# Optimization experiments

Measured on AMD Instinct MI355X. Metric: run time of the kernel, lower is better.

The kernel has to match this reference:

```python
import jax, jax.numpy as jnp
import numpy as np

NUM_HEADS = 32
NUM_KV_HEADS = 8
HEAD_DIM = 128
ROPE_THETA = 10000.0


def _rope_cos_sin(seq_len, head_dim, dtype):
    inv_freq = 1.0 / (ROPE_THETA ** (jnp.arange(0, head_dim, 2, dtype=jnp.float32) / head_dim))
    t = jnp.arange(seq_len, dtype=jnp.float32)
    freqs = jnp.outer(t, inv_freq)              # [S, hd/2]
    emb = jnp.concatenate([freqs, freqs], axis=-1)  # [S, hd]
    return jnp.cos(emb).astype(dtype), jnp.sin(emb).astype(dtype)


def _rotate_half(x):
    h = x.shape[-1] // 2
    return jnp.concatenate([-x[..., h:], x[..., :h]], axis=-1)


def _apply_rope(x, cos, sin):
    # x: [B, H, S, D]; cos/sin: [S, D] (position_ids = arange(S) in prefill)
    return x * cos[None, None] + _rotate_half(x) * sin[None, None]


def setup_inputs() -> dict:
    key = jax.random.key(0)
    ks = jax.random.split(key, 5)
    B, S, H = 1, 2048, 4096
    return {
        "hidden_states": jax.random.normal(ks[0], (B, S, H), dtype=jnp.float32),
        "Wq": jax.random.normal(ks[1], (H, NUM_HEADS * HEAD_DIM), dtype=jnp.float32) * 0.02,
        "Wk": jax.random.normal(ks[2], (H, NUM_KV_HEADS * HEAD_DIM), dtype=jnp.float32) * 0.02,
        "Wv": jax.random.normal(ks[3], (H, NUM_KV_HEADS * HEAD_DIM), dtype=jnp.float32) * 0.02,
        "Wo": jax.random.normal(ks[4], (NUM_HEADS * HEAD_DIM, H), dtype=jnp.float32) * 0.02,
    }


def reference(hidden_states, Wq, Wk, Wv, Wo):
    B, S, H = hidden_states.shape
    nh, nkv, hd = NUM_HEADS, NUM_KV_HEADS, HEAD_DIM
    groups = nh // nkv

    # fused QKV projections (bias-free, Llama-style)
    q = (hidden_states @ Wq).reshape(B, S, nh, hd).transpose(0, 2, 1, 3)   # [B,nh,S,D]
    k = (hidden_states @ Wk).reshape(B, S, nkv, hd).transpose(0, 2, 1, 3)  # [B,nkv,S,D]
    v = (hidden_states @ Wv).reshape(B, S, nkv, hd).transpose(0, 2, 1, 3)

    # inline RoPE on q and k
    cos, sin = _rope_cos_sin(S, hd, q.dtype)
    q = _apply_rope(q, cos, sin)
    k = _apply_rope(k, cos, sin)

    # GQA: repeat kv heads to match query heads (num_key_value_groups)
    k = jnp.repeat(k, groups, axis=1)  # [B,nh,S,D]
    v = jnp.repeat(v, groups, axis=1)

    scale = 1.0 / jnp.sqrt(jnp.asarray(hd, dtype=q.dtype))
    logits = jnp.einsum("bhqd,bhkd->bhqk", q, k) * scale  # [B,nh,S,S]

    # prefill causal mask (phys_past_len = 0)
    causal = jnp.tril(jnp.ones((S, S), dtype=bool))
    neg = jnp.asarray(jnp.finfo(logits.dtype).min, dtype=logits.dtype)
    logits = jnp.where(causal[None, None], logits, neg)

    attn = jax.nn.softmax(logits.astype(jnp.float32), axis=-1).astype(q.dtype)
    out = jnp.einsum("bhqk,bhkd->bhqd", attn, v)           # [B,nh,S,D]
    out = out.transpose(0, 2, 1, 3).reshape(B, S, nh * hd)  # [B,S,H]
    return out @ Wo
```

## Files before the change

### kernel.cpp

```cpp
#include <hip/hip_runtime.h>
#include <cstdint>
#include <cstddef>

typedef __attribute__((ext_vector_type(4))) float f32x4;
typedef __attribute__((ext_vector_type(16))) float f32x16;
typedef __attribute__((ext_vector_type(8))) short bf16x8;
typedef __attribute__((ext_vector_type(2))) unsigned int u32x2;

#define S_LEN   2048
#define HID     4096
#define NH      32
#define NKV     8
#define HD      128
#define QKV_N   6144

typedef const __attribute__((address_space(1))) unsigned int* gptr_t;
typedef __attribute__((address_space(3))) unsigned int* lptr_t;

__device__ __forceinline__ void gload_lds16(const void* g, void* l) {
  __builtin_amdgcn_global_load_lds((gptr_t)g, (lptr_t)l, 16, 0, 0);
}

__device__ __forceinline__ ushort f2bf(float f) {
  union { float f; uint32_t u; } v; v.f = f;
  uint32_t r = v.u + 0x7FFFu + ((v.u >> 16) & 1u);
  return (ushort)(r >> 16);
}
__device__ __forceinline__ float bf2f(ushort u) {
  union { uint32_t u; float f; } v; v.u = ((uint32_t)u) << 16;
  return v.f;
}

__global__ void prep_all(const float* __restrict__ hs,
                         const float* __restrict__ Wq, const float* __restrict__ Wk,
                         const float* __restrict__ Wv, const float* __restrict__ Wo,
                         ushort* __restrict__ hsb,
                         ushort* __restrict__ WqkvT, ushort* __restrict__ WoT) {
  int id = blockIdx.x;
  if (id < 8192) {
    int i = (id * 256 + (int)threadIdx.x) * 4;
    float4 v = *reinterpret_cast<const float4*>(hs + i);
    ushort4 o;
    o.x = f2bf(v.x); o.y = f2bf(v.y); o.z = f2bf(v.z); o.w = f2bf(v.w);
    *reinterpret_cast<ushort4*>(hsb + i) = o;
    return;
  }
  __shared__ float t[32][33];
  id -= 8192;
  const float* src; ushort* dst; int C, local;
  if (id < 16384)        { src = Wq; dst = WqkvT;                      C = 4096; local = id; }
  else if (id < 20480)   { src = Wk; dst = WqkvT + (size_t)4096 * HID; C = 1024; local = id - 16384; }
  else if (id < 24576)   { src = Wv; dst = WqkvT + (size_t)5120 * HID; C = 1024; local = id - 20480; }
  else                   { src = Wo; dst = WoT;                        C = 4096; local = id - 24576; }
  const int cb = C >> 5;
  int bx = local % cb, by = local / cb;
  int tx = threadIdx.x & 31, ty = threadIdx.x >> 5;
  int r0 = by * 32, c0 = bx * 32;
#pragma unroll
  for (int i = 0; i < 32; i += 8)
    t[ty + i][tx] = src[(size_t)(r0 + ty + i) * C + c0 + tx];
  __syncthreads();
#pragma unroll
  for (int i = 0; i < 32; i += 8)
    dst[(size_t)(c0 + ty + i) * 4096 + r0 + tx] = f2bf(t[tx][ty + i]);
}

template <bool BF16_OUT>
__global__ __launch_bounds__(256, 4) void gemm_bt(
    const ushort* __restrict__ A, const ushort* __restrict__ B,
    void* __restrict__ Cp, int M, int N, int K) {
  __shared__ ushort a_lds[128 * 64];
  __shared__ ushort b_lds[128 * 64];
  const int tid = threadIdx.x;
  const int wid = tid >> 6, lane = tid & 63;
  const int l16 = lane & 15, lk = lane >> 4;
  const int wr = wid >> 1, wc = wid & 1;
  const size_t a_row0 = (size_t)blockIdx.y * 128;
  const size_t b_row0 = (size_t)blockIdx.x * 128;

  f32x4 acc[4][4] = {};

  for (int kt = 0; kt < K; kt += 64) {
    __syncthreads();
#pragma unroll
    for (int i = 0; i < 4; ++i) {
      int c = i * 256 + tid;
      int row = c >> 3, pos = c & 7;
      int src = pos ^ (row & 7);
      gload_lds16(A + (a_row0 + row) * K + kt + src * 8, &a_lds[c * 8]);
      gload_lds16(B + (b_row0 + row) * K + kt + src * 8, &b_lds[c * 8]);
    }
    __syncthreads();

#pragma unroll
    for (int kk = 0; kk < 2; ++kk) {
      bf16x8 af[4], bf[4];
#pragma unroll
      for (int m = 0; m < 4; ++m) {
        int row = wr * 64 + m * 16 + l16;
        int ch = (kk * 4 + lk) ^ (row & 7);
        af[m] = *reinterpret_cast<const bf16x8*>(&a_lds[row * 64 + ch * 8]);
      }
#pragma unroll
      for (int n = 0; n < 4; ++n) {
        int row = wc * 64 + n * 16 + l16;
        int ch = (kk * 4 + lk) ^ (row & 7);
        bf[n] = *reinterpret_cast<const bf16x8*>(&b_lds[row * 64 + ch * 8]);
      }
#pragma unroll
      for (int m = 0; m < 4; ++m)
#pragma unroll
        for (int n = 0; n < 4; ++n)
          acc[m][n] = __builtin_amdgcn_mfma_f32_16x16x32_bf16(af[m], bf[n], acc[m][n], 0, 0, 0);
    }
  }

#pragma unroll
  for (int m = 0; m < 4; ++m) {
    int row_b = wr * 64 + m * 16 + lk * 4;
#pragma unroll
    for (int n = 0; n < 4; ++n) {
      int col = (int)b_row0 + wc * 64 + n * 16 + l16;
#pragma unroll
      for (int r = 0; r < 4; ++r) {
        size_t row = a_row0 + row_b + r;
        if constexpr (BF16_OUT)
          ((ushort*)Cp)[row * N + col] = f2bf(acc[m][n][r]);
        else
          ((float*)Cp)[row * N + col] = acc[m][n][r];
      }
    }
  }
}

__global__ __launch_bounds__(256, 4) void gemm_o_ks(
    const ushort* __restrict__ A, const ushort* __restrict__ B,
    float* __restrict__ P0, float* __restrict__ P1) {
  __shared__ ushort a_lds[128 * 64];
  __shared__ ushort b_lds[128 * 64];
  const int bid = blockIdx.x;
  const int kh = bid >> 9;
  const int rem = bid & 511;
  const size_t b_row0 = (size_t)(rem & 31) * 128;
  const size_t a_row0 = (size_t)(rem >> 5) * 128;
  const int k0 = kh * 2048, k1 = k0 + 2048;
  float* __restrict__ P = kh ? P1 : P0;
  const int tid = threadIdx.x;
  const int wid = tid >> 6, lane = tid & 63;
  const int l16 = lane & 15, lk = lane >> 4;
  const int wr = wid >> 1, wc = wid & 1;

  f32x4 acc[4][4] = {};

  for (int kt = k0; kt < k1; kt += 64) {
    __syncthreads();
#pragma unroll
    for (int i = 0; i < 4; ++i) {
      int c = i * 256 + tid;
      int row = c >> 3, pos = c & 7;
      int src = pos ^ (row & 7);
      gload_lds16(A + (a_row0 + row) * HID + kt + src * 8, &a_lds[c * 8]);
      gload_lds16(B + (b_row0 + row) * HID + kt + src * 8, &b_lds[c * 8]);
    }
    __syncthreads();

#pragma unroll
    for (int kk = 0; kk < 2; ++kk) {
      bf16x8 af[4], bf[4];
#pragma unroll
      for (int m = 0; m < 4; ++m) {
        int row = wr * 64 + m * 16 + l16;
        int ch = (kk * 4 + lk) ^ (row & 7);
        af[m] = *reinterpret_cast<const bf16x8*>(&a_lds[row * 64 + ch * 8]);
      }
#pragma unroll
      for (int n = 0; n < 4; ++n) {
        int row = wc * 64 + n * 16 + l16;
        int ch = (kk * 4 + lk) ^ (row & 7);
        bf[n] = *reinterpret_cast<const bf16x8*>(&b_lds[row * 64 + ch * 8]);
      }
#pragma unroll
      for (int m = 0; m < 4; ++m)
#pragma unroll
        for (int n = 0; n < 4; ++n)
          acc[m][n] = __builtin_amdgcn_mfma_f32_16x16x32_bf16(af[m], bf[n], acc[m][n], 0, 0, 0);
    }
  }

#pragma unroll
  for (int m = 0; m < 4; ++m) {
    int row_b = wr * 64 + m * 16 + lk * 4;
#pragma unroll
    for (int n = 0; n < 4; ++n) {
      int col = (int)b_row0 + wc * 64 + n * 16 + l16;
#pragma unroll
      for (int r = 0; r < 4; ++r)
        P[(a_row0 + row_b + r) * HID + col] = acc[m][n][r];
    }
  }
}

__global__ void add_f32(const float* __restrict__ a, const float* __restrict__ b,
                        float* __restrict__ o, int n) {
  int i = (blockIdx.x * 256 + threadIdx.x) * 4;
  if (i >= n) return;
  float4 x = *reinterpret_cast<const float4*>(a + i);
  float4 y = *reinterpret_cast<const float4*>(b + i);
  float4 z; z.x = x.x + y.x; z.y = x.y + y.y; z.z = x.z + y.z; z.w = x.w + y.w;
  *reinterpret_cast<float4*>(o + i) = z;
}

__global__ void rope_and_tv(ushort* __restrict__ QKV, ushort* __restrict__ Vt) {
  if (blockIdx.x < 2560) {
    int idx = blockIdx.x * 256 + threadIdx.x;
    int dg = idx & 7;
    int t = idx >> 3;
    int s = t / 40;
    int hh = t - s * 40;
    if (s >= S_LEN) return;
    int col = (hh < NH) ? hh * HD : HID + (hh - NH) * HD;
    ushort* base = QKV + (size_t)s * QKV_N + col + dg * 8;

    union U { uint4 v; ushort u[8]; };
    U L, H, OL, OH;
    L.v = *reinterpret_cast<const uint4*>(base);
    H.v = *reinterpret_cast<const uint4*>(base + 64);
    const float C0 = 13.287712379549449f / 64.0f;
#pragma unroll
    for (int j = 0; j < 8; ++j) {
      int d = dg * 8 + j;
      float invf = exp2f(-(float)d * C0);
      float ang = (float)s * invf;
      float sn, cs;
      sincosf(ang, &sn, &cs);
      float xl = bf2f(L.u[j]), xh = bf2f(H.u[j]);
      OL.u[j] = f2bf(xl * cs - xh * sn);
      OH.u[j] = f2bf(xh * cs + xl * sn);
    }
    *reinterpret_cast<uint4*>(base) = OL.v;
    *reinterpret_cast<uint4*>(base + 64) = OH.v;
  } else {
    __shared__ ushort t[64][65];
    int local = blockIdx.x - 2560;
    int s0 = (local & 31) * 64;
    int d0 = ((local >> 5) & 1) * 64;
    int hkv = local >> 6;
    int tx = threadIdx.x & 63, ty = threadIdx.x >> 6;
#pragma unroll
    for (int i = 0; i < 64; i += 4)
      t[i + ty][tx] = QKV[(size_t)(s0 + i + ty) * QKV_N + HID + NKV * HD + hkv * HD + d0 + tx];
    __syncthreads();
#pragma unroll
    for (int i = 0; i < 64; i += 4)
      Vt[((size_t)hkv * HD + d0 + i + ty) * S_LEN + s0 + tx] = t[tx][i + ty];
  }
}

__global__ __launch_bounds__(256, 2) void attn_kernel(
    const ushort* __restrict__ QKV, const ushort* __restrict__ Vt, ushort* __restrict__ AO) {
  constexpr float SCALE = 0.08838834764831845f;
  __shared__ ushort k_lds[2][64 * 128];
  __shared__ ushort v_lds[2][128 * 64];

  const int lin = blockIdx.x;
  const int h = ((lin & 7) << 2) + ((lin >> 3) & 3);
  const int p = lin >> 5;
  const int hkv = h >> 2;
  const int tid = threadIdx.x, wid = tid >> 6, lane = tid & 63;
  const int l32 = lane & 31;
  const int hi = lane >> 5;

  auto stageKV = [&](int buf, int kt) {
#pragma unroll
    for (int i = 0; i < 4; ++i) {
      int c = i * 256 + wid * 64 + lane;
      int row = c >> 4, ch = c & 15;
      int sch = ch ^ (row & 7);
      gload_lds16(QKV + (size_t)(kt * 64 + row) * QKV_N + HID + hkv * HD + sch * 8,
                  &k_lds[buf][c * 8]);
    }
#pragma unroll
    for (int i = 0; i < 4; ++i) {
      int c = i * 256 + wid * 64 + lane;
      int row = c >> 3, ch = c & 7;
      int sch = ch ^ (row & 7);
      gload_lds16(Vt + ((size_t)hkv * HD + row) * S_LEN + (size_t)kt * 64 + sch * 8,
                  &v_lds[buf][c * 8]);
    }
  };

  for (int pi = 0; pi < 2; ++pi) {
    const int qb = pi ? (15 - p) : p;
    const int q0 = qb * 128;
    const int qg = q0 + wid * 32 + l32;

    bf16x8 qf[8];
    {
      const ushort* qrow = QKV + (size_t)qg * QKV_N + h * HD + hi * 8;
#pragma unroll
      for (int ds = 0; ds < 8; ++ds)
        qf[ds] = *reinterpret_cast<const bf16x8*>(qrow + ds * 16);
    }

    float m_run = -1e30f, l_run = 0.f;
    f32x16 oacc[4] = {};

    stageKV(0, 0);
    __syncthreads();

    const int nt = 2 * qb + 2;
    for (int kt = 0; kt < nt; ++kt) {
      const int cur = kt & 1;
      if (kt + 1 < nt) stageKV(cur ^ 1, kt + 1);

      if (kt * 64 <= q0 + wid * 32 + 31) {
        float pv[32];
        __builtin_amdgcn_s_setprio(1);
#pragma unroll
        for (int kf = 0; kf < 2; ++kf) {
          f32x16 s = {};
          int rk = kf * 32 + l32;
#pragma unroll
          for (int ds = 0; ds < 8; ++ds) {
            int c16 = (ds * 2 + hi) ^ (rk & 7);
            bf16x8 kfr = *reinterpret_cast<const bf16x8*>(&k_lds[cur][rk * 128 + c16 * 8]);
            s = __builtin_amdgcn_mfma_f32_32x32x16_bf16(kfr, qf[ds], s, 0, 0, 0);
          }
#pragma unroll
          for (int r = 0; r < 16; ++r) pv[kf * 16 + r] = s[r] * SCALE;
        }
        __builtin_amdgcn_s_setprio(0);

        if (kt * 64 + 63 > q0 + wid * 32) {
#pragma unroll
          for (int kf = 0; kf < 2; ++kf)
#pragma unroll
            for (int r = 0; r < 16; ++r) {
              int kl = kf * 32 + (r & 3) + 8 * (r >> 2) + 4 * hi;
              if (kt * 64 + kl > qg) pv[kf * 16 + r] = -1e30f;
            }
        }

        float mt = pv[0];
#pragma unroll
        for (int i = 1; i < 32; ++i) mt = fmaxf(mt, pv[i]);
        mt = fmaxf(mt, __shfl_xor(mt, 32, 64));
        float mn = fmaxf(m_run, mt);
        float alpha = __expf(m_run - mn);
        float ls = 0.f;
#pragma unroll
        for (int i = 0; i < 32; ++i) { pv[i] = __expf(pv[i] - mn); ls += pv[i]; }
        ls += __shfl_xor(ls, 32, 64);
        l_run = l_run * alpha + ls;
        m_run = mn;
#pragma unroll
        for (int f = 0; f < 4; ++f)
#pragma unroll
          for (int r = 0; r < 16; ++r) oacc[f][r] *= alpha;

        union PW { uint32_t w[4]; bf16x8 v; } pa[4];
#pragma unroll
        for (int ks = 0; ks < 4; ++ks) {
          uint32_t x0, x1, y0, y1;
          asm("v_cvt_pk_bf16_f32 %0, %1, %2" : "=v"(x0) : "v"(pv[8 * ks + 0]), "v"(pv[8 * ks + 1]));
          asm("v_cvt_pk_bf16_f32 %0, %1, %2" : "=v"(x1) : "v"(pv[8 * ks + 2]), "v"(pv[8 * ks + 3]));
          asm("v_cvt_pk_bf16_f32 %0, %1, %2" : "=v"(y0) : "v"(pv[8 * ks + 4]), "v"(pv[8 * ks + 5]));
          asm("v_cvt_pk_bf16_f32 %0, %1, %2" : "=v"(y1) : "v"(pv[8 * ks + 6]), "v"(pv[8 * ks + 7]));
          u32x2 r0 = __builtin_amdgcn_permlane32_swap(x0, y0, false, false);
          u32x2 r1 = __builtin_amdgcn_permlane32_swap(x1, y1, false, false);
          pa[ks].w[0] = r0.x; pa[ks].w[1] = r1.x; pa[ks].w[2] = r0.y; pa[ks].w[3] = r1.y;
        }

        __builtin_amdgcn_s_setprio(1);
#pragma unroll
        for (int ks = 0; ks < 4; ++ks) {
#pragma unroll
          for (int f = 0; f < 4; ++f) {
            int dv = f * 32 + l32;
            int c8 = (2 * ks + hi) ^ (dv & 7);
            bf16x8 vfr = *reinterpret_cast<const bf16x8*>(&v_lds[cur][dv * 64 + c8 * 8]);
            oacc[f] = __builtin_amdgcn_mfma_f32_32x32x16_bf16(vfr, pa[ks].v, oacc[f], 0, 0, 0);
          }
        }
        __builtin_amdgcn_s_setprio(0);
      }

      __syncthreads();
    }

    float inv_l = 1.0f / l_run;
    ushort* aorow = AO + (size_t)qg * HID + h * HD;
#pragma unroll
    for (int f = 0; f < 4; ++f)
#pragma unroll
      for (int g = 0; g < 4; ++g) {
        ushort4 o;
        o.x = f2bf(oacc[f][g * 4 + 0] * inv_l);
        o.y = f2bf(oacc[f][g * 4 + 1] * inv_l);
        o.z = f2bf(oacc[f][g * 4 + 2] * inv_l);
        o.w = f2bf(oacc[f][g * 4 + 3] * inv_l);
        *reinterpret_cast<ushort4*>(aorow + f * 32 + g * 8 + 4 * hi) = o;
      }
  }
}

extern "C" void kernel_launch(void* const* d_in, const int* in_sizes, int n_in,
                              void* d_out, int out_size, void* d_ws, size_t ws_size,
                              hipStream_t stream) {
  (void)in_sizes; (void)n_in; (void)out_size;
  const float* hs = (const float*)d_in[0];
  const float* Wq = (const float*)d_in[1];
  const float* Wk = (const float*)d_in[2];
  const float* Wv = (const float*)d_in[3];
  const float* Wo = (const float*)d_in[4];
  float* out = (float*)d_out;

  char* ws = (char*)d_ws;
  const size_t OFF_HSB   = 0;
  const size_t OFF_WQKVT = OFF_HSB + 16777216;
  const size_t OFF_WOT   = OFF_WQKVT + 50331648;
  const size_t OFF_QKV   = OFF_WOT + 33554432;
  const size_t OFF_VT    = OFF_QKV + 25165824;
  const size_t OFF_AO    = OFF_VT + 4194304;
  if (ws_size < OFF_AO + 16777216) return;

  ushort* hsb   = (ushort*)(ws + OFF_HSB);
  ushort* WqkvT = (ushort*)(ws + OFF_WQKVT);
  ushort* WoT   = (ushort*)(ws + OFF_WOT);
  ushort* QKV   = (ushort*)(ws + OFF_QKV);
  ushort* Vt    = (ushort*)(ws + OFF_VT);
  ushort* AO    = (ushort*)(ws + OFF_AO);
  float* P0 = (float*)(ws + 0);
  float* P1 = (float*)(ws + 33554432);

  prep_all<<<49152, 256, 0, stream>>>(hs, Wq, Wk, Wv, Wo, hsb, WqkvT, WoT);
  gemm_bt<true><<<dim3(QKV_N / 128, S_LEN / 128), 256, 0, stream>>>(hsb, WqkvT, QKV, S_LEN, QKV_N, HID);
  rope_and_tv<<<3072, 256, 0, stream>>>(QKV, Vt);
  attn_kernel<<<256, 256, 0, stream>>>(QKV, Vt, AO);
  gemm_o_ks<<<1024, 256, 0, stream>>>(AO, WoT, P0, P1);
  add_f32<<<8192, 256, 0, stream>>>(P0, P1, out, S_LEN * HID);
}
```

Before: 330.2 us.

## Widen weight transpose tiles and remap GEMM blocks across XCDs

The weight transpose/convert pass now uses 64x64 tiles with float4 loads and ushort4 stores instead of 32x32 scalar accesses, which cuts the block count and issues wider memory transactions. Both GEMMs also remap block ids so that consecutive logical tiles land on the same XCD (id&7 chunking), aiming for better L2 reuse of shared A/B tiles. The padded LDS tile (69 columns) may still see some bank conflicts on the vectorized reads, and the remap assumes the block count divides by 8.

```diff
diff --git a/kernel.cpp b/kernel.cpp
--- a/kernel.cpp
+++ b/kernel.cpp
@@ -45,24 +45,36 @@
     *reinterpret_cast<ushort4*>(hsb + i) = o;
     return;
   }
-  __shared__ float t[32][33];
+  __shared__ float t[64][69];
   id -= 8192;
   const float* src; ushort* dst; int C, local;
-  if (id < 16384)        { src = Wq; dst = WqkvT;                      C = 4096; local = id; }
-  else if (id < 20480)   { src = Wk; dst = WqkvT + (size_t)4096 * HID; C = 1024; local = id - 16384; }
-  else if (id < 24576)   { src = Wv; dst = WqkvT + (size_t)5120 * HID; C = 1024; local = id - 20480; }
-  else                   { src = Wo; dst = WoT;                        C = 4096; local = id - 24576; }
-  const int cb = C >> 5;
+  if (id < 4096)        { src = Wq; dst = WqkvT;                      C = 4096; local = id; }
+  else if (id < 5120)   { src = Wk; dst = WqkvT + (size_t)4096 * HID; C = 1024; local = id - 4096; }
+  else if (id < 6144)   { src = Wv; dst = WqkvT + (size_t)5120 * HID; C = 1024; local = id - 5120; }
+  else                  { src = Wo; dst = WoT;                        C = 4096; local = id - 6144; }
+  const int cb = C >> 6;
   int bx = local % cb, by = local / cb;
-  int tx = threadIdx.x & 31, ty = threadIdx.x >> 5;
-  int r0 = by * 32, c0 = bx * 32;
-#pragma unroll
-  for (int i = 0; i < 32; i += 8)
-    t[ty + i][tx] = src[(size_t)(r0 + ty + i) * C + c0 + tx];
+  int tx = threadIdx.x & 15, ty = threadIdx.x >> 4;
+  int r0 = by * 64, c0 = bx * 64;
+#pragma unroll
+  for (int i = 0; i < 4; ++i) {
+    float4 v = *reinterpret_cast<const float4*>(&src[(size_t)(r0 + ty + i * 16) * C + c0 + tx * 4]);
+    t[ty + i * 16][tx * 4 + 0] = v.x;
+    t[ty + i * 16][tx * 4 + 1] = v.y;
+    t[ty + i * 16][tx * 4 + 2] = v.z;
+    t[ty + i * 16][tx * 4 + 3] = v.w;
+  }
   __syncthreads();
 #pragma unroll
-  for (int i = 0; i < 32; i += 8)
-    dst[(size_t)(c0 + ty + i) * 4096 + r0 + tx] = f2bf(t[tx][ty + i]);
+  for (int i = 0; i < 4; ++i) {
+    int cc = ty + i * 16;
+    ushort4 o;
+    o.x = f2bf(t[tx * 4 + 0][cc]);
+    o.y = f2bf(t[tx * 4 + 1][cc]);
+    o.z = f2bf(t[tx * 4 + 2][cc]);
+    o.w = f2bf(t[tx * 4 + 3][cc]);
+    *reinterpret_cast<ushort4*>(&dst[(size_t)(c0 + cc) * 4096 + r0 + tx * 4]) = o;
+  }
 }
 
 template <bool BF16_OUT>
@@ -75,8 +87,12 @@
   const int wid = tid >> 6, lane = tid & 63;
   const int l16 = lane & 15, lk = lane >> 4;
   const int wr = wid >> 1, wc = wid & 1;
-  const size_t a_row0 = (size_t)blockIdx.y * 128;
-  const size_t b_row0 = (size_t)blockIdx.x * 128;
+  const int nx = gridDim.x;
+  const int orig = blockIdx.y * nx + blockIdx.x;
+  const int per = (nx * gridDim.y) >> 3;
+  const int wgid = (orig & 7) * per + (orig >> 3);
+  const size_t a_row0 = (size_t)(wgid / nx) * 128;
+  const size_t b_row0 = (size_t)(wgid % nx) * 128;
 
   f32x4 acc[4][4] = {};
 
@@ -138,9 +154,10 @@
     float* __restrict__ P0, float* __restrict__ P1) {
   __shared__ ushort a_lds[128 * 64];
   __shared__ ushort b_lds[128 * 64];
-  const int bid = blockIdx.x;
-  const int kh = bid >> 9;
-  const int rem = bid & 511;
+  const int orig = blockIdx.x;
+  const int wgid = (orig & 7) * 128 + (orig >> 3);
+  const int kh = wgid >> 9;
+  const int rem = wgid & 511;
   const size_t b_row0 = (size_t)(rem & 31) * 128;
   const size_t a_row0 = (size_t)(rem >> 5) * 128;
   const int k0 = kh * 2048, k1 = k0 + 2048;
@@ -433,7 +450,7 @@
   float* P0 = (float*)(ws + 0);
   float* P1 = (float*)(ws + 33554432);
 
-  prep_all<<<49152, 256, 0, stream>>>(hs, Wq, Wk, Wv, Wo, hsb, WqkvT, WoT);
+  prep_all<<<18432, 256, 0, stream>>>(hs, Wq, Wk, Wv, Wo, hsb, WqkvT, WoT);
   gemm_bt<true><<<dim3(QKV_N / 128, S_LEN / 128), 256, 0, stream>>>(hsb, WqkvT, QKV, S_LEN, QKV_N, HID);
   rope_and_tv<<<3072, 256, 0, stream>>>(QKV, Vt);
   attn_kernel<<<256, 256, 0, stream>>>(QKV, Vt, AO);
```

New measurement: 337.1 us. +2.1%, slower.
